# Kernel tuning notes

Measured on AMD Instinct MI355X. Metric: run time of the kernel, lower is better.

The kernel has to match this reference:

```python
import jax, jax.numpy as jnp
import numpy as np

B, S, D = 2, 2048, 1024
H = 16
HD = D // H  # 64


def setup_inputs() -> dict:
    key = jax.random.key(0)
    ks = jax.random.split(key, 6)
    scale = 1.0 / np.sqrt(D)
    return {
        "x": jax.random.normal(ks[0], (B, S, D), dtype=jnp.float32),
        "W_q": jax.random.normal(ks[1], (D, D), dtype=jnp.float32) * scale,
        "W_k": jax.random.normal(ks[2], (D, D), dtype=jnp.float32) * scale,
        "W_v": jax.random.normal(ks[3], (D, D), dtype=jnp.float32) * scale,
        "W_o": jax.random.normal(ks[4], (D, D), dtype=jnp.float32) * scale,
        "b_o": jax.random.normal(ks[5], (D,), dtype=jnp.float32) * 0.01,
    }


def reference(x, W_q, W_k, W_v, W_o, b_o):
    # Projections (torch Linear applies x @ W.T; weights here stored as [out, in])
    q = jnp.einsum("bsd,ed->bse", x, W_q).reshape(B, S, H, HD)
    k = jnp.einsum("bsd,ed->bse", x, W_k).reshape(B, S, H, HD)
    v = jnp.einsum("bsd,ed->bse", x, W_v).reshape(B, S, H, HD)
    # scores: [B, H, S, S]
    scores = jnp.einsum("bqhd,bkhd->bhqk", q, k) / jnp.sqrt(jnp.float32(HD))
    attn = jax.nn.softmax(scores, axis=-1)
    # dropout is identity in eval mode
    out = jnp.einsum("bhqk,bkhd->bqhd", attn, v).reshape(B, S, D)
    return jnp.einsum("bsd,ed->bse", out, W_o) + b_o
```

## Files before the change

kernel.cpp:

```cpp
#include <hip/hip_runtime.h>
#include <hip/hip_bf16.h>

typedef __hip_bfloat16 bf16_t;
typedef __bf16 bf16x8 __attribute__((ext_vector_type(8)));
typedef __bf16 bf16x4 __attribute__((ext_vector_type(4)));
typedef short  s16x4  __attribute__((ext_vector_type(4)));
typedef float  f32x4  __attribute__((ext_vector_type(4)));

#define MFMA(a, b, c) __builtin_amdgcn_mfma_f32_16x16x32_bf16((a), (b), (c), 0, 0, 0)

__device__ __forceinline__ f32x4 mfma16(bf16x4 a, bf16x4 b, f32x4 c) {
#if __has_builtin(__builtin_amdgcn_mfma_f32_16x16x16_bf16)
  return __builtin_amdgcn_mfma_f32_16x16x16_bf16(a, b, c, 0, 0, 0);
#else
  return __builtin_amdgcn_mfma_f32_16x16x16bf16_1k(
      __builtin_bit_cast(s16x4, a), __builtin_bit_cast(s16x4, b), c, 0, 0, 0);
#endif
}

__device__ __forceinline__ bf16x8 ldg8(const bf16_t* p) {
  return *reinterpret_cast<const bf16x8*>(p);
}
__device__ __forceinline__ bf16x4 ldg4(const bf16_t* p) {
  return *reinterpret_cast<const bf16x4*>(p);
}
__device__ __forceinline__ void st8(bf16_t* p, bf16x8 v) {
  *reinterpret_cast<bf16x8*>(p) = v;
}
__device__ __forceinline__ void store_out(bf16_t* p, float v) { *p = __float2bfloat16(v); }
__device__ __forceinline__ void store_out(float* p, float v)  { *p = v; }

__device__ __forceinline__ void async16(const bf16_t* g, bf16_t* l) {
  __builtin_amdgcn_global_load_lds(
      (const __attribute__((address_space(1))) void*)g,
      (__attribute__((address_space(3))) void*)l, 16, 0, 0);
}

__global__ __launch_bounds__(256) void cvt_kernel(
    const float* __restrict__ x,  const float* __restrict__ Wq,
    const float* __restrict__ Wk, const float* __restrict__ Wv,
    const float* __restrict__ Wo,
    bf16_t* __restrict__ xb,  bf16_t* __restrict__ Wqb,
    bf16_t* __restrict__ Wkb, bf16_t* __restrict__ Wvb,
    bf16_t* __restrict__ Wob) {
  const int bid = blockIdx.x;
  const float* src; bf16_t* dst; size_t base;
  float scl = 1.0f;
  if (bid < 2048)      { src = x;  dst = xb;  base = (size_t)bid * 2048; }
  else if (bid < 2560) { src = Wq; dst = Wqb; base = (size_t)(bid - 2048) * 2048;
                         scl = 0.180336878f; }
  else if (bid < 3072) { src = Wk; dst = Wkb; base = (size_t)(bid - 2560) * 2048; }
  else if (bid < 3584) { src = Wv; dst = Wvb; base = (size_t)(bid - 3072) * 2048; }
  else                 { src = Wo; dst = Wob; base = (size_t)(bid - 3584) * 2048; }
  const size_t i0 = base + (size_t)threadIdx.x * 8;
  const float4 f0 = *reinterpret_cast<const float4*>(src + i0);
  const float4 f1 = *reinterpret_cast<const float4*>(src + i0 + 4);
  bf16x8 v;
  v[0] = (__bf16)(f0.x * scl); v[1] = (__bf16)(f0.y * scl);
  v[2] = (__bf16)(f0.z * scl); v[3] = (__bf16)(f0.w * scl);
  v[4] = (__bf16)(f1.x * scl); v[5] = (__bf16)(f1.y * scl);
  v[6] = (__bf16)(f1.z * scl); v[7] = (__bf16)(f1.w * scl);
  st8(dst + i0, v);
}

#define GK 1024

template <typename OutT, bool BIAS>
__device__ __forceinline__ void gemm_tile(
    const bf16_t* __restrict__ A, const bf16_t* __restrict__ B,
    OutT* __restrict__ C, const float* __restrict__ bias,
    int bm, int bn, int ldc, bf16_t* As, bf16_t* Bs) {
  const int tid  = threadIdx.x;
  const int lane = tid & 63;
  const int wave = tid >> 6;
  const int wm   = (wave & 1) << 6;
  const int wn   = (wave >> 1) << 6;
  const int lr   = lane & 15;
  const int lq   = lane >> 4;

  const int srow = tid >> 3;
  const int sx   = ((tid & 7) ^ (srow & 7)) << 3;

  const bf16_t* Ag = A + (size_t)(bm + srow) * GK + sx;
  const bf16_t* Bg = B + (size_t)(bn + srow) * GK + sx;
  bf16_t* Asw = As + wave * 512;
  bf16_t* Bsw = Bs + wave * 512;

  f32x4 acc[4][4];
#pragma unroll
  for (int i = 0; i < 4; ++i)
#pragma unroll
    for (int j = 0; j < 4; ++j) acc[i][j] = (f32x4){0.f, 0.f, 0.f, 0.f};

  for (int k0 = 0; k0 < GK; k0 += 64) {
    __syncthreads();
#pragma unroll
    for (int g = 0; g < 4; ++g) {
      async16(Ag + k0 + (size_t)(g * 32) * GK, Asw + g * 2048);
      async16(Bg + k0 + (size_t)(g * 32) * GK, Bsw + g * 2048);
    }
    __syncthreads();
#pragma unroll
    for (int ks = 0; ks < 2; ++ks) {
      bf16x8 af[4], bf[4];
      const int chs = ((ks * 4 + lq) ^ (lr & 7)) << 3;
#pragma unroll
      for (int i = 0; i < 4; ++i) {
        af[i] = ldg8(&As[(wm + i * 16 + lr) * 64 + chs]);
        bf[i] = ldg8(&Bs[(wn + i * 16 + lr) * 64 + chs]);
      }
#pragma unroll
      for (int mi = 0; mi < 4; ++mi)
#pragma unroll
        for (int ni = 0; ni < 4; ++ni)
          acc[mi][ni] = MFMA(af[mi], bf[ni], acc[mi][ni]);
    }
  }

#pragma unroll
  for (int ni = 0; ni < 4; ++ni) {
    const int col = bn + wn + ni * 16 + lr;
    float bv = 0.f;
    if (BIAS) bv = bias[col];
#pragma unroll
    for (int mi = 0; mi < 4; ++mi) {
#pragma unroll
      for (int r = 0; r < 4; ++r) {
        const int row = bm + wm + mi * 16 + lq * 4 + r;
        store_out(&C[(size_t)row * ldc + col], acc[mi][ni][r] + bv);
      }
    }
  }
}

__global__ __launch_bounds__(256) void qkv_kernel(
    const bf16_t* __restrict__ x, const bf16_t* __restrict__ Wq,
    const bf16_t* __restrict__ Wk, const bf16_t* __restrict__ Wv,
    bf16_t* __restrict__ Q, bf16_t* __restrict__ Kp, bf16_t* __restrict__ Vt) {
  __shared__ alignas(16) bf16_t As[128 * 64];
  __shared__ alignas(16) bf16_t Bs[128 * 64];
  const int bid = blockIdx.x;
  const int z   = blockIdx.y;
  const int mt  = (bid & 31) * 128;
  const int nt  = (bid >> 5) * 128;
  if (z == 0) {
    gemm_tile<bf16_t, false>(x, Wq, Q, nullptr, mt, nt, 1024, As, Bs);
  } else if (z == 1) {
    gemm_tile<bf16_t, false>(x, Wk, Kp, nullptr, mt, nt, 1024, As, Bs);
  } else {
    gemm_tile<bf16_t, false>(Wv, x, Vt, nullptr, nt, mt, 4096, As, Bs);
  }
}

__global__ __launch_bounds__(256) void out_proj_kernel(
    const bf16_t* __restrict__ Ao, const bf16_t* __restrict__ Wo,
    const float* __restrict__ bias, float* __restrict__ out) {
  __shared__ alignas(16) bf16_t As[128 * 64];
  __shared__ alignas(16) bf16_t Bs[128 * 64];
  const int bid = blockIdx.x;
  gemm_tile<float, true>(Ao, Wo, out, bias, (bid & 31) * 128, (bid >> 5) * 128, 1024, As, Bs);
}

#define VPAD 68

__global__ __launch_bounds__(256) void attn_kernel(
    const bf16_t* __restrict__ Q, const bf16_t* __restrict__ Kp,
    const bf16_t* __restrict__ Vt, bf16_t* __restrict__ Ao) {
  __shared__ alignas(16) char smem_raw[4 * 64 * 17 * 4];
  bf16_t* Ks = (bf16_t*)smem_raw;
  bf16_t* Vs = (bf16_t*)(smem_raw + 8192);
  float*  Osc = (float*)smem_raw;

  const int tid  = threadIdx.x;
  const int lane = tid & 63;
  const int wave = tid >> 6;
  const int lr   = lane & 15;
  const int lq   = lane >> 4;
  const int bh   = blockIdx.x;
  const int qt   = blockIdx.y;
  const int b    = bh >> 4;
  const int h    = bh & 15;
  const size_t tok0 = (size_t)b * 2048;
  const int col0 = h * 64;
  const int qblk = qt * 128 + wave * 32;

  bf16x8 qf[2][2];
#pragma unroll
  for (int nt = 0; nt < 2; ++nt) {
    const size_t qrow = tok0 + qblk + nt * 16 + lr;
#pragma unroll
    for (int c = 0; c < 2; ++c)
      qf[nt][c] = ldg8(&Q[qrow * 1024 + col0 + c * 32 + lq * 8]);
  }

  f32x4 o[2][4];
#pragma unroll
  for (int nt = 0; nt < 2; ++nt)
#pragma unroll
    for (int i = 0; i < 4; ++i) o[nt][i] = (f32x4){0.f, 0.f, 0.f, 0.f};
  float lsum[2] = {0.f, 0.f};

  const int srow = tid >> 3;
  const int sxk  = ((tid & 7) ^ (srow & 7)) << 3;
  const int sxv  = (tid & 7) << 3;
  bf16_t* Ksw = Ks + wave * 512;

  const int koff0 = lr * 64 + ((lq ^ (lr & 7)) << 3);
  const int koff1 = lr * 64 + (((lq + 4) ^ (lr & 7)) << 3);
  const int voff  = lr * VPAD + lq * 4;

  for (int kv0 = 0; kv0 < 2048; kv0 += 64) {
    const bf16_t* Kg = Kp + (tok0 + kv0) * 1024 + col0;
    const bf16_t* Vg = Vt + (size_t)col0 * 4096 + tok0 + kv0;
    const bf16x8 v0 = ldg8(Vg + (size_t)srow * 4096 + sxv);
    const bf16x8 v1 = ldg8(Vg + (size_t)(srow + 32) * 4096 + sxv);
    __syncthreads();
    async16(Kg + (size_t)srow * 1024 + sxk, Ksw);
    async16(Kg + (size_t)(srow + 32) * 1024 + sxk, Ksw + 2048);
    st8(&Vs[srow * VPAD + sxv], v0);
    st8(&Vs[(srow + 32) * VPAD + sxv], v1);
    __syncthreads();

#pragma unroll
    for (int c = 0; c < 4; ++c) {
      const bf16x8 kf0 = ldg8(&Ks[c * 1024 + koff0]);
      const bf16x8 kf1 = ldg8(&Ks[c * 1024 + koff1]);
      bf16x4 pb[2];
#pragma unroll
      for (int nt = 0; nt < 2; ++nt) {
        f32x4 sT = {0.f, 0.f, 0.f, 0.f};
        sT = MFMA(kf0, qf[nt][0], sT);
        sT = MFMA(kf1, qf[nt][1], sT);
        const float p0 = exp2f(sT.x);
        const float p1 = exp2f(sT.y);
        const float p2 = exp2f(sT.z);
        const float p3 = exp2f(sT.w);
        pb[nt][0] = (__bf16)p0; pb[nt][1] = (__bf16)p1;
        pb[nt][2] = (__bf16)p2; pb[nt][3] = (__bf16)p3;
        lsum[nt] += (p0 + p1) + (p2 + p3);
      }
#pragma unroll
      for (int ht = 0; ht < 4; ++ht) {
        const bf16x4 vf = ldg4(&Vs[ht * 16 * VPAD + voff + c * 16]);
        o[0][ht] = mfma16(vf, pb[0], o[0][ht]);
        o[1][ht] = mfma16(vf, pb[1], o[1][ht]);
      }
    }
  }

  __syncthreads();

  float* Ow = &Osc[wave * 64 * 17];
#pragma unroll
  for (int nt = 0; nt < 2; ++nt) {
    float ls = lsum[nt];
    ls += __shfl_xor(ls, 16);
    ls += __shfl_xor(ls, 32);
    const float invl = 1.f / ls;

#pragma unroll
    for (int ht = 0; ht < 4; ++ht)
#pragma unroll
      for (int r = 0; r < 4; ++r)
        Ow[(ht * 16 + lq * 4 + r) * 17 + lr] = o[nt][ht][r] * invl;

    const int qq = lane >> 2;
    const int hc = (lane & 3) * 16;
    bf16x8 w0, w1;
#pragma unroll
    for (int i = 0; i < 8; ++i) {
      w0[i] = (__bf16)Ow[(hc + i) * 17 + qq];
      w1[i] = (__bf16)Ow[(hc + 8 + i) * 17 + qq];
    }
    bf16_t* dst = Ao + (tok0 + qblk + nt * 16 + qq) * 1024 + col0 + hc;
    st8(dst, w0);
    st8(dst + 8, w1);
  }
}

extern "C" void kernel_launch(void* const* d_in, const int* in_sizes, int n_in,
                              void* d_out, int out_size, void* d_ws, size_t ws_size,
                              hipStream_t stream) {
  const float* x  = (const float*)d_in[0];
  const float* Wq = (const float*)d_in[1];
  const float* Wk = (const float*)d_in[2];
  const float* Wv = (const float*)d_in[3];
  const float* Wo = (const float*)d_in[4];
  const float* bo = (const float*)d_in[5];
  float* out = (float*)d_out;

  const size_t NTOK = 4096, DMODEL = 1024, WSZ = DMODEL * DMODEL;
  bf16_t* xb  = (bf16_t*)d_ws;
  bf16_t* Wqb = xb + NTOK * DMODEL;
  bf16_t* Wkb = Wqb + WSZ;
  bf16_t* Wvb = Wkb + WSZ;
  bf16_t* Wob = Wvb + WSZ;
  bf16_t* Q   = Wob + WSZ;
  bf16_t* Kp  = Q  + NTOK * DMODEL;
  bf16_t* Vt  = Kp + NTOK * DMODEL;
  bf16_t* Ao  = Vt + NTOK * DMODEL;

  cvt_kernel<<<dim3(4096), 256, 0, stream>>>(x, Wq, Wk, Wv, Wo, xb, Wqb, Wkb, Wvb, Wob);
  qkv_kernel<<<dim3(256, 3), 256, 0, stream>>>(xb, Wqb, Wkb, Wvb, Q, Kp, Vt);
  attn_kernel<<<dim3(32, 16), 256, 0, stream>>>(Q, Kp, Vt, Ao);
  out_proj_kernel<<<dim3(256, 1), 256, 0, stream>>>(Ao, Wob, bo, out);
}
```

Baseline: 211.0 us.

## Double-buffer K/V tiles in attention and use hardware exp2

The attention kernel now keeps two LDS buffers for K and V. The next tile's K is loaded asynchronously and V is prefetched into registers while the current tile is computed, so there is one barrier per tile instead of two and global latency is hidden behind MFMA work. exp2f is replaced with the native v_exp_f32 instruction, and launch bounds request two blocks per CU. In exchange, LDS use roughly doubles and register pressure rises, which could limit occupancy.

```diff
diff --git a/kernel.cpp b/kernel.cpp
--- a/kernel.cpp
+++ b/kernel.cpp
@@ -15,6 +15,16 @@
 #else
   return __builtin_amdgcn_mfma_f32_16x16x16bf16_1k(
       __builtin_bit_cast(s16x4, a), __builtin_bit_cast(s16x4, b), c, 0, 0, 0);
+#endif
+}
+
+__device__ __forceinline__ float fast_exp2(float x) {
+#if __has_builtin(__builtin_amdgcn_exp2f)
+  return __builtin_amdgcn_exp2f(x);
+#else
+  float r;
+  asm("v_exp_f32 %0, %1" : "=v"(r) : "v"(x));
+  return r;
 #endif
 }
 
@@ -163,12 +173,14 @@
 
 #define VPAD 68
 
-__global__ __launch_bounds__(256) void attn_kernel(
+__global__ __launch_bounds__(256, 2) void attn_kernel(
     const bf16_t* __restrict__ Q, const bf16_t* __restrict__ Kp,
     const bf16_t* __restrict__ Vt, bf16_t* __restrict__ Ao) {
-  __shared__ alignas(16) char smem_raw[4 * 64 * 17 * 4];
-  bf16_t* Ks = (bf16_t*)smem_raw;
-  bf16_t* Vs = (bf16_t*)(smem_raw + 8192);
+  __shared__ alignas(16) char smem_raw[2 * 8192 + 2 * 8704];
+  bf16_t* Ks0 = (bf16_t*)smem_raw;
+  bf16_t* Ks1 = Ks0 + 4096;
+  bf16_t* Vs0 = (bf16_t*)(smem_raw + 16384);
+  bf16_t* Vs1 = Vs0 + 64 * VPAD;
   float*  Osc = (float*)smem_raw;
 
   const int tid  = threadIdx.x;
@@ -203,48 +215,81 @@
   const int srow = tid >> 3;
   const int sxk  = ((tid & 7) ^ (srow & 7)) << 3;
   const int sxv  = (tid & 7) << 3;
-  bf16_t* Ksw = Ks + wave * 512;
+  const int kdst = wave * 512;
 
   const int koff0 = lr * 64 + ((lq ^ (lr & 7)) << 3);
   const int koff1 = lr * 64 + (((lq + 4) ^ (lr & 7)) << 3);
   const int voff  = lr * VPAD + lq * 4;
 
-  for (int kv0 = 0; kv0 < 2048; kv0 += 64) {
-    const bf16_t* Kg = Kp + (tok0 + kv0) * 1024 + col0;
-    const bf16_t* Vg = Vt + (size_t)col0 * 4096 + tok0 + kv0;
-    const bf16x8 v0 = ldg8(Vg + (size_t)srow * 4096 + sxv);
-    const bf16x8 v1 = ldg8(Vg + (size_t)(srow + 32) * 4096 + sxv);
-    __syncthreads();
-    async16(Kg + (size_t)srow * 1024 + sxk, Ksw);
-    async16(Kg + (size_t)(srow + 32) * 1024 + sxk, Ksw + 2048);
-    st8(&Vs[srow * VPAD + sxv], v0);
-    st8(&Vs[(srow + 32) * VPAD + sxv], v1);
-    __syncthreads();
-
+  const bf16_t* Kg0 = Kp + tok0 * 1024 + col0;
+  const bf16_t* Vg0 = Vt + (size_t)col0 * 4096 + tok0;
+
+  auto stage_k = [&](const bf16_t* Kg, bf16_t* Ksn) {
+    async16(Kg + (size_t)srow * 1024 + sxk, Ksn + kdst);
+    async16(Kg + (size_t)(srow + 32) * 1024 + sxk, Ksn + kdst + 2048);
+  };
+
+  auto compute_tile = [&](const bf16_t* Ksc, const bf16_t* Vsc) {
 #pragma unroll
     for (int c = 0; c < 4; ++c) {
-      const bf16x8 kf0 = ldg8(&Ks[c * 1024 + koff0]);
-      const bf16x8 kf1 = ldg8(&Ks[c * 1024 + koff1]);
+      const bf16x8 kf0 = ldg8(&Ksc[c * 1024 + koff0]);
+      const bf16x8 kf1 = ldg8(&Ksc[c * 1024 + koff1]);
       bf16x4 pb[2];
 #pragma unroll
       for (int nt = 0; nt < 2; ++nt) {
         f32x4 sT = {0.f, 0.f, 0.f, 0.f};
         sT = MFMA(kf0, qf[nt][0], sT);
         sT = MFMA(kf1, qf[nt][1], sT);
-        const float p0 = exp2f(sT.x);
-        const float p1 = exp2f(sT.y);
-        const float p2 = exp2f(sT.z);
-        const float p3 = exp2f(sT.w);
+        const float p0 = fast_exp2(sT.x);
+        const float p1 = fast_exp2(sT.y);
+        const float p2 = fast_exp2(sT.z);
+        const float p3 = fast_exp2(sT.w);
         pb[nt][0] = (__bf16)p0; pb[nt][1] = (__bf16)p1;
         pb[nt][2] = (__bf16)p2; pb[nt][3] = (__bf16)p3;
         lsum[nt] += (p0 + p1) + (p2 + p3);
       }
 #pragma unroll
       for (int ht = 0; ht < 4; ++ht) {
-        const bf16x4 vf = ldg4(&Vs[ht * 16 * VPAD + voff + c * 16]);
+        const bf16x4 vf = ldg4(&Vsc[ht * 16 * VPAD + voff + c * 16]);
         o[0][ht] = mfma16(vf, pb[0], o[0][ht]);
         o[1][ht] = mfma16(vf, pb[1], o[1][ht]);
       }
+    }
+  };
+
+  {
+    const bf16x8 v0 = ldg8(Vg0 + (size_t)srow * 4096 + sxv);
+    const bf16x8 v1 = ldg8(Vg0 + (size_t)(srow + 32) * 4096 + sxv);
+    stage_k(Kg0, Ks0);
+    st8(&Vs0[srow * VPAD + sxv], v0);
+    st8(&Vs0[(srow + 32) * VPAD + sxv], v1);
+  }
+
+#pragma unroll 1
+  for (int t = 0; t < 32; t += 2) {
+    __syncthreads();
+    {
+      const bf16_t* Kg = Kg0 + (size_t)(t + 1) * 65536;
+      const bf16_t* Vg = Vg0 + (t + 1) * 64;
+      const bf16x8 v0 = ldg8(Vg + (size_t)srow * 4096 + sxv);
+      const bf16x8 v1 = ldg8(Vg + (size_t)(srow + 32) * 4096 + sxv);
+      stage_k(Kg, Ks1);
+      compute_tile(Ks0, Vs0);
+      st8(&Vs1[srow * VPAD + sxv], v0);
+      st8(&Vs1[(srow + 32) * VPAD + sxv], v1);
+    }
+    __syncthreads();
+    if (t + 2 < 32) {
+      const bf16_t* Kg = Kg0 + (size_t)(t + 2) * 65536;
+      const bf16_t* Vg = Vg0 + (t + 2) * 64;
+      const bf16x8 v0 = ldg8(Vg + (size_t)srow * 4096 + sxv);
+      const bf16x8 v1 = ldg8(Vg + (size_t)(srow + 32) * 4096 + sxv);
+      stage_k(Kg, Ks0);
+      compute_tile(Ks1, Vs1);
+      st8(&Vs0[srow * VPAD + sxv], v0);
+      st8(&Vs0[(srow + 32) * VPAD + sxv], v1);
+    } else {
+      compute_tile(Ks1, Vs1);
     }
   }
 
```

After: 184.2 us. 1.15x faster.
